# Performance work log

Hardware: AMD Instinct MI355X
Metric: run time of the kernel (lower is better)

The kernel has to match this reference:

```python
import jax, jax.numpy as jnp
import numpy as np
import math

N_WAY, K_SHOT, Q_QUERY, PRJ_NUM, D = 5, 5, 15, 6, 64


def setup_inputs() -> dict:
    key = jax.random.key(0)
    k1, k2 = jax.random.split(key)
    feat = jax.random.normal(k1, (600, 64, 10, 10), dtype=jnp.float32)
    label = jax.random.randint(k2, (450,), 0, N_WAY)
    scale = jnp.ones((1,), dtype=jnp.float32)
    r = jnp.zeros((2,), dtype=jnp.float32)
    return {"feat": feat, "label": label, "scale": scale, "r": r}


def reference(feat, label, scale, r):
    ns = N_WAY * K_SHOT * PRJ_NUM  # 150 support images
    inv_sqrt_d = 1.0 / math.sqrt(D)
    support_xf = feat[:ns] * inv_sqrt_d
    query_xf = feat[ns:] * inv_sqrt_d
    q, c, h, w = query_xf.shape

    # support: (n_way, k_shot*prj_num*h*w, c)
    support = support_xf.reshape(N_WAY, K_SHOT * PRJ_NUM, c, h * w)
    support = jnp.transpose(support, (0, 1, 3, 2)).reshape(N_WAY, -1, c)
    # query: (q*h*w, c)
    query = jnp.transpose(query_xf.reshape(q, c, h * w), (0, 2, 1)).reshape(q * h * w, c)

    alpha, beta = r[0], r[1]
    reg = support.shape[1] / support.shape[2]
    lam = reg * jnp.exp(alpha)
    rho = jnp.exp(beta)

    # Woodbury / normal-equations path: hat = (S^T S + lam I)^-1 S^T S, per class
    sts = jnp.einsum('nkc,nkd->ncd', support, support)  # (n_way, c, c)
    m = sts + lam * jnp.eye(c, dtype=sts.dtype)[None]
    hat = jnp.linalg.inv(m) @ sts  # (n_way, c, c)

    Q_bar = jnp.einsum('qc,ncd->nqd', query, hat) * rho  # (n_way, q*h*w, c)
    dist = jnp.sum((Q_bar - query[None]) ** 2, axis=2).T  # (q*h*w, n_way)
    neg_l2_dist = -dist.reshape(q, h * w, N_WAY).mean(axis=1)  # (q, n_way)

    y_pred = jax.nn.softmax(neg_l2_dist, axis=1)
    logits = neg_l2_dist * scale[0]
    logp = jax.nn.log_softmax(logits, axis=1)
    loss = -jnp.mean(jnp.take_along_axis(logp, label[:, None], axis=1))
    return y_pred, loss
```

## Files before the change

### kernel.cpp

```cpp
#include <hip/hip_runtime.h>
#include <math.h>


typedef __attribute__((ext_vector_type(8))) short short8;
typedef __attribute__((ext_vector_type(4))) short short4v;
typedef __attribute__((ext_vector_type(4))) float f32x4;

#define NSUP 150
#define NQ 450
#define PIX 100
#define IMG_STRIDE 6400
#define MAGIC 0x5F3D2B1Cu

static __device__ __forceinline__ short bf16r(float x) {
  unsigned u = __builtin_bit_cast(unsigned, x);
  u += 0x7FFFu + ((u >> 16) & 1u);
  return (short)(u >> 16);
}
static __device__ __forceinline__ float b2f(short v) {
  return __builtin_bit_cast(float, ((unsigned)(unsigned short)v) << 16);
}
static __device__ __forceinline__ void st_flag(unsigned* p, unsigned v) {
  __builtin_amdgcn_fence(__ATOMIC_RELEASE, "agent");
  __hip_atomic_store(p, v, __ATOMIC_RELAXED, __HIP_MEMORY_SCOPE_AGENT);
}
static __device__ __forceinline__ void spin_rlx(unsigned* p) {
  int guard = 1 << 22;
  while (__hip_atomic_load(p, __ATOMIC_RELAXED, __HIP_MEMORY_SCOPE_AGENT) != MAGIC
         && --guard) __builtin_amdgcn_s_sleep(2);
}

static __device__ __forceinline__ void gram_accum(const float* __restrict__ f,
                                                  f32x4 acc[4][4], int r, int g) {
  #pragma unroll
  for (int ks = 0; ks < 4; ++ks) {
    short8 frag[4];
    const int kb = ks * 32 + g * 8;
    #pragma unroll
    for (int R = 0; R < 4; ++R) {
      short8 q;
      const float* p = f + (R * 16 + r) * PIX + kb;
      if (ks < 3) {
        float4 lo = *(const float4*)p;
        float4 hi = *(const float4*)(p + 4);
        q[0] = bf16r(lo.x); q[1] = bf16r(lo.y); q[2] = bf16r(lo.z); q[3] = bf16r(lo.w);
        q[4] = bf16r(hi.x); q[5] = bf16r(hi.y); q[6] = bf16r(hi.z); q[7] = bf16r(hi.w);
      } else if (g == 0) {
        float4 lo = *(const float4*)p;
        q[0] = bf16r(lo.x); q[1] = bf16r(lo.y); q[2] = bf16r(lo.z); q[3] = bf16r(lo.w);
        q[4] = 0; q[5] = 0; q[6] = 0; q[7] = 0;
      } else {
        #pragma unroll
        for (int j = 0; j < 8; ++j) q[j] = 0;
      }
      frag[R] = q;
    }
    #pragma unroll
    for (int R = 0; R < 4; ++R)
      #pragma unroll
      for (int C = 0; C < 4; ++C)
        acc[R][C] = __builtin_amdgcn_mfma_f32_16x16x32_bf16(frag[R], frag[C],
                                                            acc[R][C], 0, 0, 0);
  }
}

static __device__ __forceinline__ void mm64q(const short* A, const short* B,
                                             f32x4 t[2][2], int r, int g,
                                             int wr, int wc) {
  #pragma unroll
  for (int ks = 0; ks < 2; ++ks) {
    short8 af[2], bfr[2];
    #pragma unroll
    for (int i = 0; i < 2; ++i) {
      af[i]  = *(const short8*)(A + (wr * 32 + i * 16 + r) * 72 + ks * 32 + g * 8);
      bfr[i] = *(const short8*)(B + (wc * 32 + i * 16 + r) * 72 + ks * 32 + g * 8);
    }
    #pragma unroll
    for (int i = 0; i < 2; ++i)
      #pragma unroll
      for (int j = 0; j < 2; ++j)
        t[i][j] = __builtin_amdgcn_mfma_f32_16x16x32_bf16(af[i], bfr[j],
                                                          t[i][j], 0, 0, 0);
  }
}

#define ZERO_ACC4(t)                                  \
  _Pragma("unroll") for (int R = 0; R < 4; ++R)       \
  _Pragma("unroll") for (int C = 0; C < 4; ++C)       \
  _Pragma("unroll") for (int q = 0; q < 4; ++q) t[R][C][q] = 0.f;

#define ZERO_ACC2(t)                                  \
  _Pragma("unroll") for (int R = 0; R < 2; ++R)       \
  _Pragma("unroll") for (int C = 0; C < 2; ++C)       \
  _Pragma("unroll") for (int q = 0; q < 4; ++q) t[R][C][q] = 0.f;

__global__ __launch_bounds__(256) void k_fused(
    const float* __restrict__ feat, const int* __restrict__ label,
    const float* __restrict__ scale, const float* __restrict__ rvec,
    float* __restrict__ out,
    float* __restrict__ partial,
    unsigned short* __restrict__ Gneg,
    float* __restrict__ blockloss,
    unsigned* __restrict__ gflag,
    unsigned* __restrict__ sflag,
    unsigned* __restrict__ lflag) {
  __shared__ __align__(16) char smem[65536];
  const int b = blockIdx.x, tid = threadIdx.x;
  const int wave = tid >> 6, lane = tid & 63;
  const int r = lane & 15, g = lane >> 4;

  if (b < 30) {
    float (*gbuf)[4096] = (float (*)[4096])smem;
    const int cls = b / 6, jb = b % 6;
    const int ks = wave, kb = ks * 32 + g * 8;
    f32x4 acc[4][4];
    ZERO_ACC4(acc)
    #pragma unroll
    for (int im = 0; im < 5; ++im) {
      const float* f = feat + (size_t)(cls * 30 + jb * 5 + im) * IMG_STRIDE;
      short8 frag[4];
      #pragma unroll
      for (int R = 0; R < 4; ++R) {
        short8 q;
        const float* p = f + (R * 16 + r) * PIX + kb;
        if (ks < 3) {
          float4 lo = *(const float4*)p;
          float4 hi = *(const float4*)(p + 4);
          q[0] = bf16r(lo.x); q[1] = bf16r(lo.y); q[2] = bf16r(lo.z); q[3] = bf16r(lo.w);
          q[4] = bf16r(hi.x); q[5] = bf16r(hi.y); q[6] = bf16r(hi.z); q[7] = bf16r(hi.w);
        } else if (g == 0) {
          float4 lo = *(const float4*)p;
          q[0] = bf16r(lo.x); q[1] = bf16r(lo.y); q[2] = bf16r(lo.z); q[3] = bf16r(lo.w);
          q[4] = 0; q[5] = 0; q[6] = 0; q[7] = 0;
        } else {
          #pragma unroll
          for (int j = 0; j < 8; ++j) q[j] = 0;
        }
        frag[R] = q;
      }
      #pragma unroll
      for (int R = 0; R < 4; ++R)
        #pragma unroll
        for (int C = 0; C < 4; ++C)
          acc[R][C] = __builtin_amdgcn_mfma_f32_16x16x32_bf16(frag[R], frag[C],
                                                              acc[R][C], 0, 0, 0);
    }
    #pragma unroll
    for (int R = 0; R < 4; ++R)
      #pragma unroll
      for (int C = 0; C < 4; ++C)
        #pragma unroll
        for (int q = 0; q < 4; ++q) {
          const int row = R * 16 + g * 4 + q, col = C * 16 + r;
          gbuf[wave][row * 64 + col] = acc[R][C][q];
        }
    __syncthreads();
    float* outp = partial + (size_t)b * 4096;
    for (int c = tid; c < 1024; c += 256) {
      f32x4 s0 = *(const f32x4*)&gbuf[0][4 * c];
      f32x4 s1 = *(const f32x4*)&gbuf[1][4 * c];
      f32x4 s2 = *(const f32x4*)&gbuf[2][4 * c];
      f32x4 s3 = *(const f32x4*)&gbuf[3][4 * c];
      f32x4 s = s0 + s1 + s2 + s3;
      *(float4*)(outp + 4 * c) = *(float4*)&s;
    }
    __syncthreads();
    if (tid == 0) st_flag(&gflag[b], MAGIC);
    return;
  }

  if (b < 35) {
    float* Ms   = (float*)(smem);
    short* Mb   = (short*)(smem + 16640);
    short* Tb   = (short*)(smem + 25856);
    short* Xa   = (short*)(smem + 35072);
    short* Xc   = (short*)(smem + 44288);
    float* radp = (float*)(smem + 53504);
    float* scal = (float*)(smem + 54528);

    const int n = b - 30;
    const int wr = wave >> 1, wc = wave & 1;
    const float lam = 46.875f * expf(rvec[0]);
    const float rho = expf(rvec[1]);

    if (tid < 6) spin_rlx(&gflag[6 * n + tid]);
    __syncthreads();
    __builtin_amdgcn_fence(__ATOMIC_ACQUIRE, "agent");

    {
      const float* base = partial + (size_t)n * 6 * 4096;
      #pragma unroll
      for (int c0 = 0; c0 < 4; ++c0) {
        const int c = tid + c0 * 256;
        float4 s = {0.f, 0.f, 0.f, 0.f};
        #pragma unroll
        for (int p = 0; p < 6; ++p) {
          float4 v = *(const float4*)(base + p * 4096 + 4 * c);
          s.x += v.x; s.y += v.y; s.z += v.z; s.w += v.w;
        }
        const int e = 4 * c, row = e >> 6, col = e & 63;
        const float m0 = s.x * (1.f / 64.f) + ((row == col    ) ? lam : 0.f);
        const float m1 = s.y * (1.f / 64.f) + ((row == col + 1) ? lam : 0.f);
        const float m2 = s.z * (1.f / 64.f) + ((row == col + 2) ? lam : 0.f);
        const float m3 = s.w * (1.f / 64.f) + ((row == col + 3) ? lam : 0.f);
        Ms[row * 65 + col + 0] = m0;
        Ms[row * 65 + col + 1] = m1;
        Ms[row * 65 + col + 2] = m2;
        Ms[row * 65 + col + 3] = m3;
        Mb[row * 72 + col + 0] = bf16r(m0);
        Mb[row * 72 + col + 1] = bf16r(m1);
        Mb[row * 72 + col + 2] = bf16r(m2);
        Mb[row * 72 + col + 3] = bf16r(m3);
      }
    }
    __syncthreads();

    {
      const int row = tid & 63, part = tid >> 6;
      float s = 0.f;
      #pragma unroll
      for (int k = 0; k < 16; ++k) s += fabsf(Ms[row * 65 + part * 16 + k]);
      radp[part * 64 + row] = s;
    }
    __syncthreads();
    if (tid < 64) {
      const float diag = Ms[tid * 65 + tid];
      const float rad = radp[tid] + radp[64 + tid] + radp[128 + tid] +
                        radp[192 + tid] - fabsf(diag);
      float lo = diag - rad, hi = diag + rad;
      for (int off = 32; off; off >>= 1) {
        lo = fminf(lo, __shfl_down(lo, off));
        hi = fmaxf(hi, __shfl_down(hi, off));
      }
      if (tid == 0) {
        const float a = fmaxf(lo, lam);
        const float bb = hi;
        const float s = a + bb, d = bb - a;
        scal[0] = s;
        scal[1] = 8.f / (2.f * s * s - d * d);
      }
    }
    __syncthreads();
    const float s0 = scal[0], theta = scal[1];

    for (int e = tid; e < 4096; e += 256) {
      const int i = e >> 6, j = e & 63;
      Xa[i * 72 + j] = bf16r(theta * (((i == j) ? s0 : 0.f) - Ms[i * 65 + j]));
    }
    __syncthreads();

    {
      f32x4 t[2][2];
      ZERO_ACC2(t)
      mm64q(Xa, Mb, t, r, g, wr, wc);
      #pragma unroll
      for (int i = 0; i < 2; ++i)
        #pragma unroll
        for (int j = 0; j < 2; ++j)
          #pragma unroll
          for (int q = 0; q < 4; ++q) {
            const int row = wr * 32 + i * 16 + g * 4 + q;
            const int col = wc * 32 + j * 16 + r;
            Tb[row * 72 + col] = bf16r(t[i][j][q]);
          }
    }
    __syncthreads();
    {
      f32x4 t[2][2];
      ZERO_ACC2(t)
      mm64q(Tb, Xa, t, r, g, wr, wc);
      #pragma unroll
      for (int i = 0; i < 2; ++i)
        #pragma unroll
        for (int j = 0; j < 2; ++j)
          #pragma unroll
          for (int q = 0; q < 4; ++q) {
            const int row = wr * 32 + i * 16 + g * 4 + q;
            const int col = wc * 32 + j * 16 + r;
            const int idx = row * 72 + col;
            Xc[idx] = bf16r(2.f * b2f(Xa[idx]) - t[i][j][q]);
          }
    }
    __syncthreads();
    {
      f32x4 t[2][2];
      ZERO_ACC2(t)
      mm64q(Xc, Mb, t, r, g, wr, wc);
      #pragma unroll
      for (int i = 0; i < 2; ++i)
        #pragma unroll
        for (int j = 0; j < 2; ++j)
          #pragma unroll
          for (int q = 0; q < 4; ++q) {
            const int row = wr * 32 + i * 16 + g * 4 + q;
            const int col = wc * 32 + j * 16 + r;
            Tb[row * 72 + col] = bf16r(t[i][j][q]);
          }
    }
    __syncthreads();
    {
      f32x4 t[2][2];
      ZERO_ACC2(t)
      mm64q(Tb, Xc, t, r, g, wr, wc);
      #pragma unroll
      for (int i = 0; i < 2; ++i)
        #pragma unroll
        for (int j = 0; j < 2; ++j)
          #pragma unroll
          for (int q = 0; q < 4; ++q) {
            const int row = wr * 32 + i * 16 + g * 4 + q;
            const int col = wc * 32 + j * 16 + r;
            const int idx = row * 72 + col;
            const float x2 = 2.f * b2f(Xc[idx]) - t[i][j][q];
            Xa[idx] = bf16r(((row == col) ? (rho - 1.f) : 0.f) - rho * lam * x2);
          }
    }
    __syncthreads();
    {
      f32x4 t[2][2];
      ZERO_ACC2(t)
      mm64q(Xa, Xa, t, r, g, wr, wc);
      #pragma unroll
      for (int i = 0; i < 2; ++i)
        #pragma unroll
        for (int j = 0; j < 2; ++j)
          #pragma unroll
          for (int q = 0; q < 4; ++q) {
            const int row = wr * 32 + i * 16 + g * 4 + q;
            const int col = wc * 32 + j * 16 + r;
            Gneg[n * 4096 + row * 64 + col] =
                (unsigned short)bf16r(t[i][j][q] * (-0.01f));
          }
    }
    __syncthreads();
    if (tid == 0) st_flag(&sflag[n], MAGIC);
    return;
  }

  const int img = (b - 35) * 4 + wave;
  const bool ok = img < NQ;
  const float sc = scale[0];
  const int lab = ok ? label[img] : 0;
  f32x4 acc[4][4];
  ZERO_ACC4(acc)
  if (ok)
    gram_accum(feat + (size_t)(NSUP + img) * IMG_STRIDE, acc, r, g);

  if (tid < 5) spin_rlx(&sflag[tid]);
  __syncthreads();
  __builtin_amdgcn_fence(__ATOMIC_ACQUIRE, "agent");

  unsigned short* Gs = (unsigned short*)smem;
  for (int e = tid; e < 5120; e += 256) {
    const int e4 = e * 4;
    const int nn = e4 >> 12, rem = e4 & 4095, row = rem >> 6, col = rem & 63;
    *(short4v*)&Gs[nn * 4352 + row * 68 + col] = *(const short4v*)&Gneg[e4];
  }
  __syncthreads();

  float myloss = 0.f;
  float nl[5] = {0.f, 0.f, 0.f, 0.f, 0.f};
  if (ok) {
    #pragma unroll
    for (int R = 0; R < 4; ++R)
      #pragma unroll
      for (int C = 0; C < 4; ++C)
        #pragma unroll
        for (int q = 0; q < 4; ++q) {
          const int row = R * 16 + g * 4 + q, col = C * 16 + r;
          const float cv = acc[R][C][q] * (1.f / 64.f);
          const int idx = row * 68 + col;
          #pragma unroll
          for (int nn = 0; nn < 5; ++nn)
            nl[nn] += b2f((short)Gs[nn * 4352 + idx]) * cv;
        }
    #pragma unroll
    for (int nn = 0; nn < 5; ++nn)
      for (int off = 32; off; off >>= 1) nl[nn] += __shfl_down(nl[nn], off);

    if (lane == 0) {
      float mx = nl[0];
      #pragma unroll
      for (int nn = 1; nn < 5; ++nn) mx = fmaxf(mx, nl[nn]);
      float ex[5], se = 0.f;
      #pragma unroll
      for (int nn = 0; nn < 5; ++nn) { ex[nn] = expf(nl[nn] - mx); se += ex[nn]; }
      const float inv = 1.f / se;
      #pragma unroll
      for (int nn = 0; nn < 5; ++nn) out[img * 5 + nn] = ex[nn] * inv;

      float mx2 = nl[0] * sc;
      #pragma unroll
      for (int nn = 1; nn < 5; ++nn) mx2 = fmaxf(mx2, nl[nn] * sc);
      float se2 = 0.f;
      #pragma unroll
      for (int nn = 0; nn < 5; ++nn) se2 += expf(nl[nn] * sc - mx2);
      myloss = mx2 + logf(se2) - nl[lab] * sc;
    }
  }

  float* wl = (float*)(smem + 43584);
  if (lane == 0) wl[wave] = ok ? myloss : 0.f;
  __syncthreads();
  if (tid == 0) {
    blockloss[b - 35] = wl[0] + wl[1] + wl[2] + wl[3];
    st_flag(&lflag[b - 35], MAGIC);
  }

  if (b == 35 && wave == 0) {
    for (int i = lane; i < 113; i += 64) spin_rlx(&lflag[i]);
    __builtin_amdgcn_fence(__ATOMIC_ACQUIRE, "agent");
    float s = 0.f;
    for (int i = lane; i < 113; i += 64) s += blockloss[i];
    for (int off = 32; off; off >>= 1) s += __shfl_down(s, off);
    if (lane == 0) out[2250] = s / 450.f;
  }
}

extern "C" void kernel_launch(void* const* d_in, const int* in_sizes, int n_in,
                              void* d_out, int out_size, void* d_ws, size_t ws_size,
                              hipStream_t stream) {
  const float* feat  = (const float*)d_in[0];
  const int*   label = (const int*)d_in[1];
  const float* scale = (const float*)d_in[2];
  const float* rvec  = (const float*)d_in[3];
  float* out = (float*)d_out;

  char* ws = (char*)d_ws;
  float*          partial   = (float*)ws;
  unsigned short* Gneg      = (unsigned short*)(ws + 491520);
  float*          blockloss = (float*)(ws + 532480);
  unsigned*       flags     = (unsigned*)(ws + 532992);
  unsigned* gflag = flags;
  unsigned* sflag = flags + 32;
  unsigned* lflag = flags + 64;

  k_fused<<<dim3(148), dim3(256), 0, stream>>>(feat, label, scale, rvec, out,
                                               partial, Gneg, blockloss,
                                               gflag, sflag, lflag);
}
```

Baseline: 24.58 us.

## Split query gram across two waves per image and fold solver into gram blocks

Query images are now processed by two waves each, with each wave covering half of the K-slices, so the grid grows to 255 blocks and every wave does half the MFMA and load work. Per-class partial distances are combined through shared memory before the softmax and loss. The five solver blocks are removed: gram blocks 0-4 go on to run the class solve after posting their flag, which cuts the block count for that stage. In exchange there are more blocks that spin on flags, a longer final loss reduction (225 entries), and the solver now waits behind its own gram work.

```diff
diff --git a/kernel.cpp b/kernel.cpp
--- a/kernel.cpp
+++ b/kernel.cpp
@@ -30,38 +30,35 @@
          && --guard) __builtin_amdgcn_s_sleep(2);
 }
 
-static __device__ __forceinline__ void gram_accum(const float* __restrict__ f,
-                                                  f32x4 acc[4][4], int r, int g) {
+static __device__ __forceinline__ void gram_ks(const float* __restrict__ f,
+                                               f32x4 acc[4][4], int ks, int r, int g) {
+  short8 frag[4];
+  const int kb = ks * 32 + g * 8;
   #pragma unroll
-  for (int ks = 0; ks < 4; ++ks) {
-    short8 frag[4];
-    const int kb = ks * 32 + g * 8;
-    #pragma unroll
-    for (int R = 0; R < 4; ++R) {
-      short8 q;
-      const float* p = f + (R * 16 + r) * PIX + kb;
-      if (ks < 3) {
-        float4 lo = *(const float4*)p;
-        float4 hi = *(const float4*)(p + 4);
-        q[0] = bf16r(lo.x); q[1] = bf16r(lo.y); q[2] = bf16r(lo.z); q[3] = bf16r(lo.w);
-        q[4] = bf16r(hi.x); q[5] = bf16r(hi.y); q[6] = bf16r(hi.z); q[7] = bf16r(hi.w);
-      } else if (g == 0) {
-        float4 lo = *(const float4*)p;
-        q[0] = bf16r(lo.x); q[1] = bf16r(lo.y); q[2] = bf16r(lo.z); q[3] = bf16r(lo.w);
-        q[4] = 0; q[5] = 0; q[6] = 0; q[7] = 0;
-      } else {
-        #pragma unroll
-        for (int j = 0; j < 8; ++j) q[j] = 0;
-      }
-      frag[R] = q;
-    }
-    #pragma unroll
-    for (int R = 0; R < 4; ++R)
-      #pragma unroll
-      for (int C = 0; C < 4; ++C)
-        acc[R][C] = __builtin_amdgcn_mfma_f32_16x16x32_bf16(frag[R], frag[C],
-                                                            acc[R][C], 0, 0, 0);
-  }
+  for (int R = 0; R < 4; ++R) {
+    short8 q;
+    const float* p = f + (R * 16 + r) * PIX + kb;
+    if (ks < 3) {
+      float4 lo = *(const float4*)p;
+      float4 hi = *(const float4*)(p + 4);
+      q[0] = bf16r(lo.x); q[1] = bf16r(lo.y); q[2] = bf16r(lo.z); q[3] = bf16r(lo.w);
+      q[4] = bf16r(hi.x); q[5] = bf16r(hi.y); q[6] = bf16r(hi.z); q[7] = bf16r(hi.w);
+    } else if (g == 0) {
+      float4 lo = *(const float4*)p;
+      q[0] = bf16r(lo.x); q[1] = bf16r(lo.y); q[2] = bf16r(lo.z); q[3] = bf16r(lo.w);
+      q[4] = 0; q[5] = 0; q[6] = 0; q[7] = 0;
+    } else {
+      #pragma unroll
+      for (int j = 0; j < 8; ++j) q[j] = 0;
+    }
+    frag[R] = q;
+  }
+  #pragma unroll
+  for (int R = 0; R < 4; ++R)
+    #pragma unroll
+    for (int C = 0; C < 4; ++C)
+      acc[R][C] = __builtin_amdgcn_mfma_f32_16x16x32_bf16(frag[R], frag[C],
+                                                          acc[R][C], 0, 0, 0);
 }
 
 static __device__ __forceinline__ void mm64q(const short* A, const short* B,
@@ -112,39 +109,12 @@
   if (b < 30) {
     float (*gbuf)[4096] = (float (*)[4096])smem;
     const int cls = b / 6, jb = b % 6;
-    const int ks = wave, kb = ks * 32 + g * 8;
+    const int ks = wave;
     f32x4 acc[4][4];
     ZERO_ACC4(acc)
     #pragma unroll
-    for (int im = 0; im < 5; ++im) {
-      const float* f = feat + (size_t)(cls * 30 + jb * 5 + im) * IMG_STRIDE;
-      short8 frag[4];
-      #pragma unroll
-      for (int R = 0; R < 4; ++R) {
-        short8 q;
-        const float* p = f + (R * 16 + r) * PIX + kb;
-        if (ks < 3) {
-          float4 lo = *(const float4*)p;
-          float4 hi = *(const float4*)(p + 4);
-          q[0] = bf16r(lo.x); q[1] = bf16r(lo.y); q[2] = bf16r(lo.z); q[3] = bf16r(lo.w);
-          q[4] = bf16r(hi.x); q[5] = bf16r(hi.y); q[6] = bf16r(hi.z); q[7] = bf16r(hi.w);
-        } else if (g == 0) {
-          float4 lo = *(const float4*)p;
-          q[0] = bf16r(lo.x); q[1] = bf16r(lo.y); q[2] = bf16r(lo.z); q[3] = bf16r(lo.w);
-          q[4] = 0; q[5] = 0; q[6] = 0; q[7] = 0;
-        } else {
-          #pragma unroll
-          for (int j = 0; j < 8; ++j) q[j] = 0;
-        }
-        frag[R] = q;
-      }
-      #pragma unroll
-      for (int R = 0; R < 4; ++R)
-        #pragma unroll
-        for (int C = 0; C < 4; ++C)
-          acc[R][C] = __builtin_amdgcn_mfma_f32_16x16x32_bf16(frag[R], frag[C],
-                                                              acc[R][C], 0, 0, 0);
-    }
+    for (int im = 0; im < 5; ++im)
+      gram_ks(feat + (size_t)(cls * 30 + jb * 5 + im) * IMG_STRIDE, acc, ks, r, g);
     #pragma unroll
     for (int R = 0; R < 4; ++R)
       #pragma unroll
@@ -166,10 +136,8 @@
     }
     __syncthreads();
     if (tid == 0) st_flag(&gflag[b], MAGIC);
-    return;
-  }
-
-  if (b < 35) {
+    if (b >= 5) return;
+
     float* Ms   = (float*)(smem);
     short* Mb   = (short*)(smem + 16640);
     short* Tb   = (short*)(smem + 25856);
@@ -178,7 +146,7 @@
     float* radp = (float*)(smem + 53504);
     float* scal = (float*)(smem + 54528);
 
-    const int n = b - 30;
+    const int n = b;
     const int wr = wave >> 1, wc = wave & 1;
     const float lam = 46.875f * expf(rvec[0]);
     const float rho = expf(rvec[1]);
@@ -337,14 +305,19 @@
     return;
   }
 
-  const int img = (b - 35) * 4 + wave;
-  const bool ok = img < NQ;
+  const int qb = b - 30;
+  const int half = wave >> 1;
+  const int img = qb * 2 + half;
   const float sc = scale[0];
-  const int lab = ok ? label[img] : 0;
+  const int lab = label[img];
   f32x4 acc[4][4];
   ZERO_ACC4(acc)
-  if (ok)
-    gram_accum(feat + (size_t)(NSUP + img) * IMG_STRIDE, acc, r, g);
+  {
+    const float* fq = feat + (size_t)(NSUP + img) * IMG_STRIDE;
+    const int ksb = (wave & 1) * 2;
+    gram_ks(fq, acc, ksb, r, g);
+    gram_ks(fq, acc, ksb + 1, r, g);
+  }
 
   if (tid < 5) spin_rlx(&sflag[tid]);
   __syncthreads();
@@ -358,60 +331,66 @@
   }
   __syncthreads();
 
-  float myloss = 0.f;
   float nl[5] = {0.f, 0.f, 0.f, 0.f, 0.f};
-  if (ok) {
-    #pragma unroll
-    for (int R = 0; R < 4; ++R)
-      #pragma unroll
-      for (int C = 0; C < 4; ++C)
-        #pragma unroll
-        for (int q = 0; q < 4; ++q) {
-          const int row = R * 16 + g * 4 + q, col = C * 16 + r;
-          const float cv = acc[R][C][q] * (1.f / 64.f);
-          const int idx = row * 68 + col;
-          #pragma unroll
-          for (int nn = 0; nn < 5; ++nn)
-            nl[nn] += b2f((short)Gs[nn * 4352 + idx]) * cv;
-        }
+  #pragma unroll
+  for (int R = 0; R < 4; ++R)
+    #pragma unroll
+    for (int C = 0; C < 4; ++C)
+      #pragma unroll
+      for (int q = 0; q < 4; ++q) {
+        const int row = R * 16 + g * 4 + q, col = C * 16 + r;
+        const float cv = acc[R][C][q] * (1.f / 64.f);
+        const int idx = row * 68 + col;
+        #pragma unroll
+        for (int nn = 0; nn < 5; ++nn)
+          nl[nn] += b2f((short)Gs[nn * 4352 + idx]) * cv;
+      }
+  #pragma unroll
+  for (int nn = 0; nn < 5; ++nn)
+    for (int off = 32; off; off >>= 1) nl[nn] += __shfl_down(nl[nn], off);
+
+  float* wl  = (float*)(smem + 43520);
+  float* wl2 = (float*)(smem + 43600);
+  if (lane == 0) {
+    #pragma unroll
+    for (int nn = 0; nn < 5; ++nn) wl[wave * 5 + nn] = nl[nn];
+  }
+  __syncthreads();
+  if ((wave & 1) == 0 && lane == 0) {
+    float nlf[5];
     #pragma unroll
     for (int nn = 0; nn < 5; ++nn)
-      for (int off = 32; off; off >>= 1) nl[nn] += __shfl_down(nl[nn], off);
-
-    if (lane == 0) {
-      float mx = nl[0];
-      #pragma unroll
-      for (int nn = 1; nn < 5; ++nn) mx = fmaxf(mx, nl[nn]);
-      float ex[5], se = 0.f;
-      #pragma unroll
-      for (int nn = 0; nn < 5; ++nn) { ex[nn] = expf(nl[nn] - mx); se += ex[nn]; }
-      const float inv = 1.f / se;
-      #pragma unroll
-      for (int nn = 0; nn < 5; ++nn) out[img * 5 + nn] = ex[nn] * inv;
-
-      float mx2 = nl[0] * sc;
-      #pragma unroll
-      for (int nn = 1; nn < 5; ++nn) mx2 = fmaxf(mx2, nl[nn] * sc);
-      float se2 = 0.f;
-      #pragma unroll
-      for (int nn = 0; nn < 5; ++nn) se2 += expf(nl[nn] * sc - mx2);
-      myloss = mx2 + logf(se2) - nl[lab] * sc;
-    }
-  }
-
-  float* wl = (float*)(smem + 43584);
-  if (lane == 0) wl[wave] = ok ? myloss : 0.f;
+      nlf[nn] = wl[wave * 5 + nn] + wl[(wave + 1) * 5 + nn];
+
+    float mx = nlf[0];
+    #pragma unroll
+    for (int nn = 1; nn < 5; ++nn) mx = fmaxf(mx, nlf[nn]);
+    float ex[5], se = 0.f;
+    #pragma unroll
+    for (int nn = 0; nn < 5; ++nn) { ex[nn] = expf(nlf[nn] - mx); se += ex[nn]; }
+    const float inv = 1.f / se;
+    #pragma unroll
+    for (int nn = 0; nn < 5; ++nn) out[img * 5 + nn] = ex[nn] * inv;
+
+    float mx2 = nlf[0] * sc;
+    #pragma unroll
+    for (int nn = 1; nn < 5; ++nn) mx2 = fmaxf(mx2, nlf[nn] * sc);
+    float se2 = 0.f;
+    #pragma unroll
+    for (int nn = 0; nn < 5; ++nn) se2 += expf(nlf[nn] * sc - mx2);
+    wl2[half] = mx2 + logf(se2) - nlf[lab] * sc;
+  }
   __syncthreads();
   if (tid == 0) {
-    blockloss[b - 35] = wl[0] + wl[1] + wl[2] + wl[3];
-    st_flag(&lflag[b - 35], MAGIC);
-  }
-
-  if (b == 35 && wave == 0) {
-    for (int i = lane; i < 113; i += 64) spin_rlx(&lflag[i]);
+    blockloss[qb] = wl2[0] + wl2[1];
+    st_flag(&lflag[qb], MAGIC);
+  }
+
+  if (qb == 0 && wave == 0) {
+    for (int i = lane; i < 225; i += 64) spin_rlx(&lflag[i]);
     __builtin_amdgcn_fence(__ATOMIC_ACQUIRE, "agent");
     float s = 0.f;
-    for (int i = lane; i < 113; i += 64) s += blockloss[i];
+    for (int i = lane; i < 225; i += 64) s += blockloss[i];
     for (int off = 32; off; off >>= 1) s += __shfl_down(s, off);
     if (lane == 0) out[2250] = s / 450.f;
   }
@@ -430,12 +409,12 @@
   float*          partial   = (float*)ws;
   unsigned short* Gneg      = (unsigned short*)(ws + 491520);
   float*          blockloss = (float*)(ws + 532480);
-  unsigned*       flags     = (unsigned*)(ws + 532992);
+  unsigned*       flags     = (unsigned*)(ws + 533504);
   unsigned* gflag = flags;
   unsigned* sflag = flags + 32;
   unsigned* lflag = flags + 64;
 
-  k_fused<<<dim3(148), dim3(256), 0, stream>>>(feat, label, scale, rvec, out,
+  k_fused<<<dim3(255), dim3(256), 0, stream>>>(feat, label, scale, rvec, out,
                                                partial, Gneg, blockloss,
                                                gflag, sflag, lflag);
 }
```

Measured after the change: 28.06 us. 1.14x slower.
